# Optimization experiments

Hardware: AMD Instinct MI355X
Metric: run time of the kernel (lower is better)

The kernel has to match this reference:

```python
import jax, jax.numpy as jnp
import numpy as np
import math

N = 100_000   # nodes
E = 1_600_000 # edges (avg degree 16)
IN = 128      # in_channels
H, C = 4, 32  # heads, out_channels (H*C = 128)
ED = 16       # edge_dim


def setup_inputs() -> dict:
    key = jax.random.key(0)
    ks = jax.random.split(key, 12)
    s = 0.02
    return {
        "x": jax.random.normal(ks[0], (N, IN), jnp.float32),
        "edge_attr": jax.random.normal(ks[1], (E, ED), jnp.float32),
        "edge_index": jax.random.randint(ks[2], (2, E), 0, N, dtype=jnp.int32),
        "Wq": jax.random.normal(ks[3], (IN, H * C), jnp.float32) * s,
        "bq": jnp.zeros((H * C,), jnp.float32),
        "Wk": jax.random.normal(ks[4], (IN, H * C), jnp.float32) * s,
        "bk": jnp.zeros((H * C,), jnp.float32),
        "Wv": jax.random.normal(ks[5], (IN, H * C), jnp.float32) * s,
        "bv": jnp.zeros((H * C,), jnp.float32),
        "We": jax.random.normal(ks[6], (ED, H * C), jnp.float32) * s,
        "Wskip": jax.random.normal(ks[7], (IN, H * C), jnp.float32) * s,
        "bskip": jnp.zeros((H * C,), jnp.float32),
        "Wbeta": jax.random.normal(ks[8], (3 * H * C, 1), jnp.float32) * s,
    }


def reference(x, edge_attr, edge_index, Wq, bq, Wk, bk, Wv, bv, We, Wskip, bskip, Wbeta):
    n = x.shape[0]
    q = (x @ Wq + bq).reshape(n, H, C)
    k = (x @ Wk + bk).reshape(n, H, C)
    v = (x @ Wv + bv).reshape(n, H, C)

    row, col = edge_index[0], edge_index[1]  # dst (target), src (source)

    # per-edge attention logits, with edge-feature fusion into keys
    k_j = k[col] + (edge_attr @ We).reshape(-1, H, C)   # [E, H, C]
    alpha = jnp.einsum("ehc,ehc->eh", q[row], k_j) / math.sqrt(C)  # [E, H]

    # scatter softmax over each destination node's neighborhood.
    # Original code stabilizes by subtracting a per-group constant via a
    m = jnp.zeros((n, H), alpha.dtype).at[row].set(alpha)  # per-group constant
    ex = jnp.exp(alpha - m[row])                            # [E, H]
    denom = jax.ops.segment_sum(ex, row, num_segments=n)    # [N, H]
    alpha = ex / (denom[row] + 1e-16)

    # weighted scatter-add aggregation of values
    msgs = v[col] * alpha[..., None]                        # [E, H, C]
    out = jax.ops.segment_sum(msgs, row, num_segments=n)    # [N, H, C]
    out = out.reshape(n, H * C)                             # concat heads

    # gated skip connection (root_weight + beta)
    x_skip = x @ Wskip + bskip                              # [N, H*C]
    beta = jax.nn.sigmoid(
        jnp.concatenate([out, x_skip, out - x_skip], axis=-1) @ Wbeta
    )                                                       # [N, 1]
    return beta * x_skip + (1.0 - beta) * out
```

## Files before the change

### kernel.cpp

```cpp
#include <hip/hip_runtime.h>
#include <stdint.h>

typedef unsigned int uint;
typedef unsigned short ushort;

typedef __attribute__((ext_vector_type(8))) short bf16x8;
typedef __attribute__((ext_vector_type(16))) float f32x16;
typedef __attribute__((ext_vector_type(4))) int   i32x4;
typedef __attribute__((ext_vector_type(4))) float f32x4;
typedef __attribute__((ext_vector_type(2))) uint  u32x2;

__device__ inline float bflo(uint u) {
    union { uint x; float f; } z; z.x = u << 16; return z.f;
}
__device__ inline float bfhi(uint u) {
    union { uint x; float f; } z; z.x = u & 0xffff0000u; return z.f;
}
__device__ inline ushort f2bf(float f) {
    union { float f; uint u; } x; x.f = f;
    uint r = (x.u + 0x7fffu + ((x.u >> 16) & 1u)) >> 16;
    return (ushort)r;
}

__global__ __launch_bounds__(256) void pack_x(const float* __restrict__ x,
                                              uint4* __restrict__ xfrag,
                                              int n, int nchunks)
{
    int o = blockIdx.x * 256 + threadIdx.x;
    if (o >= nchunks) return;
    int m    = o & 127;
    int kb   = (o >> 7) & 15;
    int tile = o >> 11;
    int row  = tile * 128 + m;
    float4 lo = make_float4(0.f, 0.f, 0.f, 0.f);
    float4 hi = make_float4(0.f, 0.f, 0.f, 0.f);
    if (row < n) {
        lo = *(const float4*)&x[(size_t)row * 128 + kb * 8];
        hi = *(const float4*)&x[(size_t)row * 128 + kb * 8 + 4];
    }
    uint4 ov;
    ov.x = (uint)f2bf(lo.x) | ((uint)f2bf(lo.y) << 16);
    ov.y = (uint)f2bf(lo.z) | ((uint)f2bf(lo.w) << 16);
    ov.z = (uint)f2bf(hi.x) | ((uint)f2bf(hi.y) << 16);
    ov.w = (uint)f2bf(hi.z) | ((uint)f2bf(hi.w) << 16);
    xfrag[o] = ov;
}

__global__ __launch_bounds__(256) void pack_w(
    const float* __restrict__ W0, const float* __restrict__ W1,
    const float* __restrict__ W2, const float* __restrict__ W3,
    const float* __restrict__ We, const float* __restrict__ bq,
    uint4* __restrict__ wfrag, float* __restrict__ btbuf)
{
    int o = blockIdx.x * 256 + threadIdx.x;
    if (o >= 10240) return;
    float v[8];
    if (o < 8192) {
        int nn = o & 127;
        int kb = (o >> 7) & 15;
        int j  = o >> 11;
        const float* W = (j == 0) ? W0 : (j == 1) ? W1 : (j == 2) ? W2 : W3;
        #pragma unroll
        for (int i = 0; i < 8; ++i) v[i] = W[(size_t)(kb * 8 + i) * 128 + nn];
    } else {
        int o2 = o - 8192;
        int nn = o2 & 127;
        int kb = (o2 >> 7) & 15;
        #pragma unroll
        for (int i = 0; i < 8; ++i) v[i] = 0.f;
        if (nn < 64) {
            int h = nn >> 4, d = nn & 15;
            const float* wq = W0 + h * 32;
            const float* we = We + (size_t)d * 128 + h * 32;
            #pragma unroll
            for (int i = 0; i < 8; ++i) {
                int k = kb * 8 + i;
                float s = 0.f;
                for (int c = 0; c < 32; ++c)
                    s += wq[(size_t)k * 128 + c] * we[c];
                v[i] = s;
            }
            if (kb == 0) {
                float s = 0.f;
                for (int c = 0; c < 32; ++c) s += bq[h * 32 + c] * we[c];
                btbuf[nn] = s;
            }
        }
    }
    uint4 ov;
    ov.x = (uint)f2bf(v[0]) | ((uint)f2bf(v[1]) << 16);
    ov.y = (uint)f2bf(v[2]) | ((uint)f2bf(v[3]) << 16);
    ov.z = (uint)f2bf(v[4]) | ((uint)f2bf(v[5]) << 16);
    ov.w = (uint)f2bf(v[6]) | ((uint)f2bf(v[7]) << 16);
    wfrag[o] = ov;
}

__global__ __launch_bounds__(256) void lin_mfma(
    const uint4* __restrict__ xfrag, const uint4* __restrict__ wfrag,
    const float* __restrict__ bq, const float* __restrict__ bk,
    const float* __restrict__ bv, const float* __restrict__ bs,
    const float* __restrict__ bt,
    uint* __restrict__ qout, uint* __restrict__ kvout, uint* __restrict__ sout,
    uint* __restrict__ tout, int n)
{
    const int tile = blockIdx.x;
    const int w  = threadIdx.x >> 6;
    const int l  = threadIdx.x & 63;
    const int lm = l & 31, lh = l >> 5;

    bf16x8 a[8];
    const uint4* ap = xfrag + (size_t)tile * 2048 + lh * 128 + w * 32 + lm;
    #pragma unroll
    for (int ks = 0; ks < 8; ++ks) a[ks] = *(const bf16x8*)(ap + ks * 256);

    const int rowbase = tile * 128 + w * 32 + 4 * lh;

    #pragma unroll
    for (int j = 0; j < 5; ++j) {
        const float* bias = (j == 0) ? bq : (j == 1) ? bk : (j == 2) ? bv
                          : (j == 3) ? bs : bt;
        uint* dst; int stride, cbase;
        if (j == 0)      { dst = qout;  stride = 64;  cbase = 0;  }
        else if (j == 1) { dst = kvout; stride = 128; cbase = 0;  }
        else if (j == 2) { dst = kvout; stride = 128; cbase = 64; }
        else if (j == 3) { dst = sout;  stride = 64;  cbase = 0;  }
        else             { dst = tout;  stride = 32;  cbase = 0;  }
        const int npc = (j == 4) ? 1 : 2;

        #pragma unroll
        for (int np = 0; np < npc; ++np) {
            const uint4* bp0 = wfrag + (size_t)j * 2048 + lh * 128 + (np * 2) * 32 + lm;
            f32x16 c0, c1;
            #pragma unroll
            for (int i = 0; i < 16; ++i) { c0[i] = 0.f; c1[i] = 0.f; }
            #pragma unroll
            for (int ks = 0; ks < 8; ++ks) {
                bf16x8 B0 = *(const bf16x8*)(bp0 + ks * 256);
                bf16x8 B1 = *(const bf16x8*)(bp0 + 32 + ks * 256);
                c0 = __builtin_amdgcn_mfma_f32_32x32x16_bf16(a[ks], B0, c0, 0, 0, 0);
                c1 = __builtin_amdgcn_mfma_f32_32x32x16_bf16(a[ks], B1, c1, 0, 0, 0);
            }
            #pragma unroll
            for (int t = 0; t < 2; ++t) {
                f32x16 cc = t ? c1 : c0;
                int gc = (np * 2 + t) * 32 + lm;
                float bl = bias[gc];
                #pragma unroll
                for (int r = 0; r < 16; ++r) {
                    float val = cc[r] + bl;
                    float partner = __shfl_xor(val, 1);
                    int gr = rowbase + (r & 3) + 8 * (r >> 2);
                    if (!(lm & 1) && gr < n) {
                        uint pk = (uint)f2bf(val) | ((uint)f2bf(partner) << 16);
                        dst[(size_t)gr * stride + cbase + (gc >> 1)] = pk;
                    }
                }
            }
        }
    }
}

__global__ __launch_bounds__(256) void hist_g_kernel(
    const int* __restrict__ rows, const float* __restrict__ ea,
    const uint* __restrict__ tb, int* __restrict__ counts,
    int* __restrict__ rank, u32x2* __restrict__ gbuf, int e)
{
    int i = blockIdx.x * blockDim.x + threadIdx.x;
    if (i >= e) return;
    int r = rows[i];
    int rk = atomicAdd(&counts[r], 1);

    const f32x4* ep = (const f32x4*)&ea[(size_t)i * 16];
    f32x4 e0 = __builtin_nontemporal_load(ep);
    f32x4 e1 = __builtin_nontemporal_load(ep + 1);
    f32x4 e2 = __builtin_nontemporal_load(ep + 2);
    f32x4 e3 = __builtin_nontemporal_load(ep + 3);
    const uint* tp = tb + (size_t)r * 32;
    float g[4];
    #pragma unroll
    for (int h = 0; h < 4; ++h) {
        uint4 ua = *(const uint4*)(tp + h * 8);
        uint4 ub = *(const uint4*)(tp + h * 8 + 4);
        g[h] = e0[0] * bflo(ua.x) + e0[1] * bfhi(ua.x)
             + e0[2] * bflo(ua.y) + e0[3] * bfhi(ua.y)
             + e1[0] * bflo(ua.z) + e1[1] * bfhi(ua.z)
             + e1[2] * bflo(ua.w) + e1[3] * bfhi(ua.w)
             + e2[0] * bflo(ub.x) + e2[1] * bfhi(ub.x)
             + e2[2] * bflo(ub.y) + e2[3] * bfhi(ub.y)
             + e3[0] * bflo(ub.z) + e3[1] * bfhi(ub.z)
             + e3[2] * bflo(ub.w) + e3[3] * bfhi(ub.w);
    }
    u32x2 gp;
    gp.x = (uint)f2bf(g[0]) | ((uint)f2bf(g[1]) << 16);
    gp.y = (uint)f2bf(g[2]) | ((uint)f2bf(g[3]) << 16);
    gbuf[i] = gp;
    rank[i] = rk;
}

__global__ __launch_bounds__(1024) void scan1_kernel(int* __restrict__ data,
                                                     int* __restrict__ bsum, int n)
{
    __shared__ int s[1024];
    int i = blockIdx.x * 1024 + threadIdx.x;
    int v = (i < n) ? data[i] : 0;
    s[threadIdx.x] = v;
    __syncthreads();
    for (int offd = 1; offd < 1024; offd <<= 1) {
        int add = (threadIdx.x >= offd) ? s[threadIdx.x - offd] : 0;
        __syncthreads();
        s[threadIdx.x] += add;
        __syncthreads();
    }
    if (i < n) data[i] = s[threadIdx.x];
    if (threadIdx.x == 1023) bsum[blockIdx.x] = s[1023];
}

__global__ __launch_bounds__(1024) void scan23_kernel(const int* __restrict__ incl,
                                                      const int* __restrict__ bsum,
                                                      int* __restrict__ offsets,
                                                      int n, int nb)
{
    __shared__ int s[1024];
    int tid = threadIdx.x;
    int v = (tid < nb) ? bsum[tid] : 0;
    s[tid] = v;
    __syncthreads();
    for (int o = 1; o < 1024; o <<= 1) {
        int add = (tid >= o) ? s[tid - o] : 0;
        __syncthreads();
        s[tid] += add;
        __syncthreads();
    }
    int bofs = (blockIdx.x == 0) ? 0 : s[blockIdx.x - 1];
    int i = blockIdx.x * 1024 + tid;
    if (i == 0) offsets[0] = 0;
    if (i < n) offsets[i + 1] = incl[i] + bofs;
}

__global__ __launch_bounds__(256) void scatter_kernel(
    const int* __restrict__ rows, const int* __restrict__ cols,
    const int* __restrict__ rank, const u32x2* __restrict__ gbuf,
    const int* __restrict__ offsets, i32x4* __restrict__ csr, int e)
{
    int i = blockIdx.x * blockDim.x + threadIdx.x;
    if (i >= e) return;
    int r = rows[i];
    int pos = offsets[r] + rank[i];
    u32x2 g = gbuf[i];
    i32x4 rec;
    rec.x = cols[i];
    rec.y = 0;
    rec.z = (int)g.x;
    rec.w = (int)g.y;
    __builtin_nontemporal_store(rec, &csr[pos]);
}

__global__ __launch_bounds__(256) void agg_kernel(
    const uint* __restrict__ qb, const uint* __restrict__ kv,
    const uint* __restrict__ sb, const i32x4* __restrict__ csr,
    const int* __restrict__ offsets, const float* __restrict__ Wbeta,
    float* __restrict__ out, int n)
{
    int wid = (blockIdx.x * blockDim.x + threadIdx.x) >> 6;
    int lane = threadIdx.x & 63;
    if (wid >= n) return;
    const int es = lane >> 4;
    const int h  = (lane >> 2) & 3;
    const int cq = lane & 3;
    const int c0 = h * 32 + cq * 8;

    uint4 uq = *(const uint4*)&qb[(size_t)wid * 64 + h * 16 + cq * 4];
    float qv[8] = { bflo(uq.x), bfhi(uq.x), bflo(uq.y), bfhi(uq.y),
                    bflo(uq.z), bfhi(uq.z), bflo(uq.w), bfhi(uq.w) };

    const int beg = offsets[wid], end = offsets[wid + 1];
    const float scale = 0.17677669529663687f;

    float denom = 0.f;
    float acc[8];
    #pragma unroll
    for (int j = 0; j < 8; ++j) acc[j] = 0.f;

    for (int i = beg; i < end; i += 8) {
        int idxA = i + es;
        int idxB = i + es + 4;
        bool vA = idxA < end;
        bool vB = idxB < end;
        int cA = vA ? idxA : end - 1;
        int cB = vB ? idxB : end - 1;
        i32x4 seA = __builtin_nontemporal_load(&csr[cA]);
        i32x4 seB = __builtin_nontemporal_load(&csr[cB]);
        const uint* krA = kv + (size_t)seA.x * 128 + h * 16 + cq * 4;
        const uint* krB = kv + (size_t)seB.x * 128 + h * 16 + cq * 4;
        uint4 kpA = *(const uint4*)krA;
        uint4 vpA = *(const uint4*)(krA + 64);
        uint4 kpB = *(const uint4*)krB;
        uint4 vpB = *(const uint4*)(krB + 64);

        uint gwA = (h & 2) ? (uint)seA.w : (uint)seA.z;
        float ghA = (h & 1) ? bfhi(gwA) : bflo(gwA);
        uint gwB = (h & 2) ? (uint)seB.w : (uint)seB.z;
        float ghB = (h & 1) ? bfhi(gwB) : bflo(gwB);

        float pa = qv[0] * bflo(kpA.x) + qv[1] * bfhi(kpA.x)
                 + qv[2] * bflo(kpA.y) + qv[3] * bfhi(kpA.y)
                 + qv[4] * bflo(kpA.z) + qv[5] * bfhi(kpA.z)
                 + qv[6] * bflo(kpA.w) + qv[7] * bfhi(kpA.w);
        float pb = qv[0] * bflo(kpB.x) + qv[1] * bfhi(kpB.x)
                 + qv[2] * bflo(kpB.y) + qv[3] * bfhi(kpB.y)
                 + qv[4] * bflo(kpB.z) + qv[5] * bfhi(kpB.z)
                 + qv[6] * bflo(kpB.w) + qv[7] * bfhi(kpB.w);
        pa += __shfl_xor(pa, 1);
        pa += __shfl_xor(pa, 2);
        pb += __shfl_xor(pb, 1);
        pb += __shfl_xor(pb, 2);
        float eA = vA ? __expf((pa + ghA) * scale) : 0.f;
        float eB = vB ? __expf((pb + ghB) * scale) : 0.f;
        denom += eA + eB;
        acc[0] += eA * bflo(vpA.x) + eB * bflo(vpB.x);
        acc[1] += eA * bfhi(vpA.x) + eB * bfhi(vpB.x);
        acc[2] += eA * bflo(vpA.y) + eB * bflo(vpB.y);
        acc[3] += eA * bfhi(vpA.y) + eB * bfhi(vpB.y);
        acc[4] += eA * bflo(vpA.z) + eB * bflo(vpB.z);
        acc[5] += eA * bfhi(vpA.z) + eB * bfhi(vpB.z);
        acc[6] += eA * bflo(vpA.w) + eB * bflo(vpB.w);
        acc[7] += eA * bfhi(vpA.w) + eB * bfhi(vpB.w);
    }

    denom += __shfl_xor(denom, 16);
    denom += __shfl_xor(denom, 32);
    #pragma unroll
    for (int j = 0; j < 8; ++j) {
        acc[j] += __shfl_xor(acc[j], 16);
        acc[j] += __shfl_xor(acc[j], 32);
    }

    float inv = 1.f / (denom + 1e-16f);
    float o[8];
    #pragma unroll
    for (int j = 0; j < 8; ++j) o[j] = acc[j] * inv;

    uint4 us = *(const uint4*)&sb[(size_t)wid * 64 + h * 16 + cq * 4];
    float xsv[8] = { bflo(us.x), bfhi(us.x), bflo(us.y), bfhi(us.y),
                     bflo(us.z), bfhi(us.z), bflo(us.w), bfhi(us.w) };

    f32x4 wb0a = *(const f32x4*)&Wbeta[c0];
    f32x4 wb0b = *(const f32x4*)&Wbeta[c0 + 4];
    f32x4 wb1a = *(const f32x4*)&Wbeta[128 + c0];
    f32x4 wb1b = *(const f32x4*)&Wbeta[128 + c0 + 4];
    f32x4 wb2a = *(const f32x4*)&Wbeta[256 + c0];
    f32x4 wb2b = *(const f32x4*)&Wbeta[256 + c0 + 4];

    float bp = 0.f;
    #pragma unroll
    for (int j = 0; j < 4; ++j) {
        bp += o[j]     * wb0a[j] + xsv[j]     * wb1a[j] + (o[j]     - xsv[j])     * wb2a[j];
        bp += o[j + 4] * wb0b[j] + xsv[j + 4] * wb1b[j] + (o[j + 4] - xsv[j + 4]) * wb2b[j];
    }
    bp += __shfl_xor(bp, 1);
    bp += __shfl_xor(bp, 2);
    bp += __shfl_xor(bp, 4);
    bp += __shfl_xor(bp, 8);
    float beta = 1.f / (1.f + __expf(-bp));

    if (es == 0) {
        float r[8];
        #pragma unroll
        for (int j = 0; j < 8; ++j) r[j] = beta * xsv[j] + (1.f - beta) * o[j];
        f32x4 r0 = { r[0], r[1], r[2], r[3] };
        f32x4 r1 = { r[4], r[5], r[6], r[7] };
        __builtin_nontemporal_store(r0, (f32x4*)&out[(size_t)wid * 128 + c0]);
        __builtin_nontemporal_store(r1, (f32x4*)&out[(size_t)wid * 128 + c0 + 4]);
    }
}

extern "C" void kernel_launch(void* const* d_in, const int* in_sizes, int n_in,
                              void* d_out, int out_size, void* d_ws, size_t ws_size,
                              hipStream_t stream)
{
    const float* x     = (const float*)d_in[0];
    const float* ea    = (const float*)d_in[1];
    const int*   ei    = (const int*)d_in[2];
    const float* Wq    = (const float*)d_in[3];
    const float* bq    = (const float*)d_in[4];
    const float* Wk    = (const float*)d_in[5];
    const float* bk    = (const float*)d_in[6];
    const float* Wv    = (const float*)d_in[7];
    const float* bv    = (const float*)d_in[8];
    const float* We    = (const float*)d_in[9];
    const float* Wsk   = (const float*)d_in[10];
    const float* bsk   = (const float*)d_in[11];
    const float* Wbeta = (const float*)d_in[12];
    float* out = (float*)d_out;

    const int N = in_sizes[0] / 128;
    const int E = in_sizes[1] / 16;
    const int NT = (N + 127) / 128;
    const int nchunks = NT * 2048;

    char* base = (char*)d_ws;
    size_t off = 0;
    auto alloc = [&](size_t bytes) -> void* {
        void* p = base + off;
        off += (bytes + 255) & ~(size_t)255;
        return p;
    };
    int*    tmp     = (int*)alloc((size_t)N * 4);
    int*    offsets = (int*)alloc((size_t)(N + 1) * 4);
    int*    bsum    = (int*)alloc(4096 * 4);
    int*    rank    = (int*)alloc((size_t)E * 4);
    u32x2*  gbuf    = (u32x2*)alloc((size_t)E * 8);
    float*  btbuf   = (float*)alloc(256);
    size_t  xfrag_bytes = (size_t)nchunks * 16;
    size_t  csr_bytes   = (size_t)E * 16;
    char*   shared_reg  = (char*)alloc(xfrag_bytes > csr_bytes ? xfrag_bytes : csr_bytes);
    uint4*  xfrag   = (uint4*)shared_reg;
    i32x4*  csr     = (i32x4*)shared_reg;
    uint4*  wfrag   = (uint4*)alloc((size_t)10240 * 16);
    uint*   qbuf    = (uint*)alloc((size_t)N * 64 * 4);
    uint*   sbuf    = (uint*)alloc((size_t)N * 64 * 4);
    uint*   tbuf    = (uint*)alloc((size_t)N * 32 * 4);
    uint*   kvbuf   = (uint*)alloc((size_t)N * 128 * 4);
    (void)ws_size; (void)n_in; (void)out_size;

    hipMemsetAsync(tmp, 0, (size_t)N * 4, stream);

    pack_x<<<(nchunks + 255) / 256, 256, 0, stream>>>(x, xfrag, N, nchunks);
    pack_w<<<40, 256, 0, stream>>>(Wq, Wk, Wv, Wsk, We, bq, wfrag, btbuf);
    lin_mfma<<<NT, 256, 0, stream>>>(xfrag, wfrag, bq, bk, bv, bsk, btbuf,
                                     qbuf, kvbuf, sbuf, tbuf, N);
    hist_g_kernel<<<(E + 255) / 256, 256, 0, stream>>>(ei, ea, tbuf, tmp,
                                                       rank, gbuf, E);
    int nb = (N + 1023) / 1024;
    scan1_kernel<<<nb, 1024, 0, stream>>>(tmp, bsum, N);
    scan23_kernel<<<nb, 1024, 0, stream>>>(tmp, bsum, offsets, N, nb);
    scatter_kernel<<<(E + 255) / 256, 256, 0, stream>>>(ei, ei + E, rank, gbuf,
                                                        offsets, csr, E);
    agg_kernel<<<(N + 3) / 4, 256, 0, stream>>>(qbuf, kvbuf, sbuf, csr,
                                                offsets, Wbeta, out, N);
}
```

Baseline: 577.4 us.

## Merge prep kernels and stage lin_mfma outputs through LDS for coalesced stores

The x packing, weight packing and counts zeroing (previously a memset) are folded into a single prep kernel, removing two launches. In lin_mfma, each MFMA output tile is written to a shared-memory buffer and then stored to global memory as full 16-byte rows, replacing the strided 4-byte stores that needed a shuffle. This aims to cut launch overhead and uncoalesced write traffic in the projection stage. The cost is about 33KB of LDS per block, which can lower occupancy, plus two barriers per output group.

After: 540.6 us. -6.4%, faster.

```diff
diff --git a/kernel.cpp b/kernel.cpp
--- a/kernel.cpp
+++ b/kernel.cpp
@@ -22,77 +22,79 @@
     return (ushort)r;
 }
 
-__global__ __launch_bounds__(256) void pack_x(const float* __restrict__ x,
-                                              uint4* __restrict__ xfrag,
-                                              int n, int nchunks)
-{
-    int o = blockIdx.x * 256 + threadIdx.x;
-    if (o >= nchunks) return;
-    int m    = o & 127;
-    int kb   = (o >> 7) & 15;
-    int tile = o >> 11;
-    int row  = tile * 128 + m;
-    float4 lo = make_float4(0.f, 0.f, 0.f, 0.f);
-    float4 hi = make_float4(0.f, 0.f, 0.f, 0.f);
-    if (row < n) {
-        lo = *(const float4*)&x[(size_t)row * 128 + kb * 8];
-        hi = *(const float4*)&x[(size_t)row * 128 + kb * 8 + 4];
-    }
-    uint4 ov;
-    ov.x = (uint)f2bf(lo.x) | ((uint)f2bf(lo.y) << 16);
-    ov.y = (uint)f2bf(lo.z) | ((uint)f2bf(lo.w) << 16);
-    ov.z = (uint)f2bf(hi.x) | ((uint)f2bf(hi.y) << 16);
-    ov.w = (uint)f2bf(hi.z) | ((uint)f2bf(hi.w) << 16);
-    xfrag[o] = ov;
-}
-
-__global__ __launch_bounds__(256) void pack_w(
+__global__ __launch_bounds__(256) void prep_kernel(
+    const float* __restrict__ x, uint4* __restrict__ xfrag, int n, int nchunks,
     const float* __restrict__ W0, const float* __restrict__ W1,
     const float* __restrict__ W2, const float* __restrict__ W3,
     const float* __restrict__ We, const float* __restrict__ bq,
-    uint4* __restrict__ wfrag, float* __restrict__ btbuf)
+    uint4* __restrict__ wfrag, float* __restrict__ btbuf,
+    int* __restrict__ counts)
 {
     int o = blockIdx.x * 256 + threadIdx.x;
-    if (o >= 10240) return;
-    float v[8];
-    if (o < 8192) {
-        int nn = o & 127;
-        int kb = (o >> 7) & 15;
-        int j  = o >> 11;
-        const float* W = (j == 0) ? W0 : (j == 1) ? W1 : (j == 2) ? W2 : W3;
-        #pragma unroll
-        for (int i = 0; i < 8; ++i) v[i] = W[(size_t)(kb * 8 + i) * 128 + nn];
-    } else {
-        int o2 = o - 8192;
-        int nn = o2 & 127;
-        int kb = (o2 >> 7) & 15;
-        #pragma unroll
-        for (int i = 0; i < 8; ++i) v[i] = 0.f;
-        if (nn < 64) {
-            int h = nn >> 4, d = nn & 15;
-            const float* wq = W0 + h * 32;
-            const float* we = We + (size_t)d * 128 + h * 32;
-            #pragma unroll
-            for (int i = 0; i < 8; ++i) {
-                int k = kb * 8 + i;
-                float s = 0.f;
-                for (int c = 0; c < 32; ++c)
-                    s += wq[(size_t)k * 128 + c] * we[c];
-                v[i] = s;
-            }
-            if (kb == 0) {
-                float s = 0.f;
-                for (int c = 0; c < 32; ++c) s += bq[h * 32 + c] * we[c];
-                btbuf[nn] = s;
+    if (o < nchunks) {
+        int m    = o & 127;
+        int kb   = (o >> 7) & 15;
+        int tile = o >> 11;
+        int row  = tile * 128 + m;
+        float4 lo = make_float4(0.f, 0.f, 0.f, 0.f);
+        float4 hi = make_float4(0.f, 0.f, 0.f, 0.f);
+        if (row < n) {
+            lo = *(const float4*)&x[(size_t)row * 128 + kb * 8];
+            hi = *(const float4*)&x[(size_t)row * 128 + kb * 8 + 4];
+        }
+        uint4 ov;
+        ov.x = (uint)f2bf(lo.x) | ((uint)f2bf(lo.y) << 16);
+        ov.y = (uint)f2bf(lo.z) | ((uint)f2bf(lo.w) << 16);
+        ov.z = (uint)f2bf(hi.x) | ((uint)f2bf(hi.y) << 16);
+        ov.w = (uint)f2bf(hi.z) | ((uint)f2bf(hi.w) << 16);
+        xfrag[o] = ov;
+        return;
+    }
+    int ow = o - nchunks;
+    if (ow < 10240) {
+        float v[8];
+        if (ow < 8192) {
+            int nn = ow & 127;
+            int kb = (ow >> 7) & 15;
+            int j  = ow >> 11;
+            const float* W = (j == 0) ? W0 : (j == 1) ? W1 : (j == 2) ? W2 : W3;
+            #pragma unroll
+            for (int i = 0; i < 8; ++i) v[i] = W[(size_t)(kb * 8 + i) * 128 + nn];
+        } else {
+            int o2 = ow - 8192;
+            int nn = o2 & 127;
+            int kb = (o2 >> 7) & 15;
+            #pragma unroll
+            for (int i = 0; i < 8; ++i) v[i] = 0.f;
+            if (nn < 64) {
+                int h = nn >> 4, d = nn & 15;
+                const float* wq = W0 + h * 32;
+                const float* we = We + (size_t)d * 128 + h * 32;
+                #pragma unroll
+                for (int i = 0; i < 8; ++i) {
+                    int k = kb * 8 + i;
+                    float s = 0.f;
+                    for (int c = 0; c < 32; ++c)
+                        s += wq[(size_t)k * 128 + c] * we[c];
+                    v[i] = s;
+                }
+                if (kb == 0) {
+                    float s = 0.f;
+                    for (int c = 0; c < 32; ++c) s += bq[h * 32 + c] * we[c];
+                    btbuf[nn] = s;
+                }
             }
         }
-    }
-    uint4 ov;
-    ov.x = (uint)f2bf(v[0]) | ((uint)f2bf(v[1]) << 16);
-    ov.y = (uint)f2bf(v[2]) | ((uint)f2bf(v[3]) << 16);
-    ov.z = (uint)f2bf(v[4]) | ((uint)f2bf(v[5]) << 16);
-    ov.w = (uint)f2bf(v[6]) | ((uint)f2bf(v[7]) << 16);
-    wfrag[o] = ov;
+        uint4 ov;
+        ov.x = (uint)f2bf(v[0]) | ((uint)f2bf(v[1]) << 16);
+        ov.y = (uint)f2bf(v[2]) | ((uint)f2bf(v[3]) << 16);
+        ov.z = (uint)f2bf(v[4]) | ((uint)f2bf(v[5]) << 16);
+        ov.w = (uint)f2bf(v[6]) | ((uint)f2bf(v[7]) << 16);
+        wfrag[ow] = ov;
+        return;
+    }
+    int z = ow - 10240;
+    if (z < n) counts[z] = 0;
 }
 
 __global__ __launch_bounds__(256) void lin_mfma(
@@ -103,6 +105,8 @@
     uint* __restrict__ qout, uint* __restrict__ kvout, uint* __restrict__ sout,
     uint* __restrict__ tout, int n)
 {
+    __shared__ ushort lt[128][130];
+
     const int tile = blockIdx.x;
     const int w  = threadIdx.x >> 6;
     const int l  = threadIdx.x & 63;
@@ -112,8 +116,6 @@
     const uint4* ap = xfrag + (size_t)tile * 2048 + lh * 128 + w * 32 + lm;
     #pragma unroll
     for (int ks = 0; ks < 8; ++ks) a[ks] = *(const bf16x8*)(ap + ks * 256);
-
-    const int rowbase = tile * 128 + w * 32 + 4 * lh;
 
     #pragma unroll
     for (int j = 0; j < 5; ++j) {
@@ -147,16 +149,38 @@
                 float bl = bias[gc];
                 #pragma unroll
                 for (int r = 0; r < 16; ++r) {
-                    float val = cc[r] + bl;
-                    float partner = __shfl_xor(val, 1);
-                    int gr = rowbase + (r & 3) + 8 * (r >> 2);
-                    if (!(lm & 1) && gr < n) {
-                        uint pk = (uint)f2bf(val) | ((uint)f2bf(partner) << 16);
-                        dst[(size_t)gr * stride + cbase + (gc >> 1)] = pk;
-                    }
+                    int lr = w * 32 + 4 * lh + (r & 3) + 8 * (r >> 2);
+                    lt[lr][gc] = f2bf(cc[r] + bl);
                 }
             }
         }
+        __syncthreads();
+        if (j != 4) {
+            int ch = threadIdx.x & 15;
+            int rr = threadIdx.x >> 4;
+            #pragma unroll
+            for (int g = 0; g < 8; ++g) {
+                int row = g * 16 + rr;
+                int gr = tile * 128 + row;
+                if (gr < n) {
+                    uint4 vls = *(const uint4*)&lt[row][ch * 8];
+                    *(uint4*)(dst + (size_t)gr * stride + cbase + ch * 4) = vls;
+                }
+            }
+        } else {
+            int ch = threadIdx.x & 7;
+            int rr = threadIdx.x >> 3;
+            #pragma unroll
+            for (int g = 0; g < 4; ++g) {
+                int row = g * 32 + rr;
+                int gr = tile * 128 + row;
+                if (gr < n) {
+                    uint4 vls = *(const uint4*)&lt[row][ch * 8];
+                    *(uint4*)(dst + (size_t)gr * stride + ch * 4) = vls;
+                }
+            }
+        }
+        __syncthreads();
     }
 }
 
@@ -423,10 +447,9 @@
     uint*   kvbuf   = (uint*)alloc((size_t)N * 128 * 4);
     (void)ws_size; (void)n_in; (void)out_size;
 
-    hipMemsetAsync(tmp, 0, (size_t)N * 4, stream);
-
-    pack_x<<<(nchunks + 255) / 256, 256, 0, stream>>>(x, xfrag, N, nchunks);
-    pack_w<<<40, 256, 0, stream>>>(Wq, Wk, Wv, Wsk, We, bq, wfrag, btbuf);
+    int prep_total = nchunks + 10240 + N;
+    prep_kernel<<<(prep_total + 255) / 256, 256, 0, stream>>>(
+        x, xfrag, N, nchunks, Wq, Wk, Wv, Wsk, We, bq, wfrag, btbuf, tmp);
     lin_mfma<<<NT, 256, 0, stream>>>(xfrag, wfrag, bq, bk, bv, bsk, btbuf,
                                      qbuf, kvbuf, sbuf, tbuf, N);
     hist_g_kernel<<<(E + 255) / 256, 256, 0, stream>>>(ei, ea, tbuf, tmp,
```
